# Kernel optimization log

Hardware: AMD Instinct MI355X
Metric: run time of the kernel (lower is better)

The kernel has to match this reference:

```python
import jax, jax.numpy as jnp
import numpy as np


def _mlp2(x, W1, b1, W2, b2):
    # two-layer MLP with ReLU hidden activation
    h = jax.nn.relu(jnp.einsum('...i,ij->...j', x, W1) + b1)
    return jnp.einsum('...i,ij->...j', h, W2) + b2


def setup_inputs() -> dict:
    key = jax.random.key(0)
    ks = jax.random.split(key, 8)
    B, N, D = 8, 256, 64
    positions = jax.random.normal(ks[0], (B, N, 3), dtype=jnp.float32)
    values = jax.random.normal(ks[1], (B, N, D), dtype=jnp.float32)
    # value_net: 2 -> D -> D ; score_net: D -> D -> 1 (He-style init)
    Wv1 = jax.random.normal(ks[2], (2, D), dtype=jnp.float32) * np.sqrt(2.0 / 2)
    bv1 = jnp.zeros((D,), dtype=jnp.float32)
    Wv2 = jax.random.normal(ks[3], (D, D), dtype=jnp.float32) * np.sqrt(2.0 / D)
    bv2 = jnp.zeros((D,), dtype=jnp.float32)
    Ws1 = jax.random.normal(ks[4], (D, D), dtype=jnp.float32) * np.sqrt(2.0 / D)
    bs1 = jnp.zeros((D,), dtype=jnp.float32)
    Ws2 = jax.random.normal(ks[5], (D, 1), dtype=jnp.float32) * np.sqrt(2.0 / D)
    bs2 = jnp.zeros((1,), dtype=jnp.float32)
    return dict(positions=positions, values=values, Wv1=Wv1, bv1=bv1, Wv2=Wv2,
                bv2=bv2, Ws1=Ws1, bs1=bs1, Ws2=Ws2, bs2=bs2)


def reference(positions, values, Wv1, bv1, Wv2, bv2, Ws1, bs1, Ws2, bs2):
    # rank-2 geometric algebra attention, reduce=True, merge_fun=join_fun='mean'
    B, N, _ = positions.shape
    r_i = positions[:, :, None, :]            # [B, N, 1, 3]
    r_j = positions[:, None, :, :]            # [B, 1, N, 3]
    # geometric product of two vectors -> scalar (dot) + bivector (wedge)
    dot = jnp.sum(r_i * r_j, axis=-1)         # [B, N, N] scalar part
    wedge = jnp.cross(r_i, r_j)               # [B, N, N, 3] bivector components
    biv_norm = jnp.sqrt(jnp.sum(wedge * wedge, axis=-1) + 1e-20)
    invariants = jnp.stack([dot, biv_norm], axis=-1)             # [B, N, N, 2]
    # merge_fun='mean' over the pair of node values
    merged = 0.5 * (values[:, :, None, :] + values[:, None, :, :])  # [B,N,N,D]
    invar_values = _mlp2(invariants, Wv1, bv1, Wv2, bv2)            # [B,N,N,D]
    # join_fun='mean' of value_net(invariants) and merged node values
    joined = 0.5 * (invar_values + merged)                          # [B,N,N,D]
    scores = _mlp2(joined, Ws1, bs1, Ws2, bs2)                      # [B,N,N,1]
    # reduce=True: softmax over all N*N product indices, output is [B, D]
    attn = jax.nn.softmax(scores.reshape(B, N * N), axis=-1).reshape(B, N, N, 1)
    output = jnp.sum(attn * joined, axis=(1, 2))                    # [B, D]
    return output
```

## Files before the change

kernel.cpp:

```cpp
#include <hip/hip_runtime.h>
#include <hip/hip_bf16.h>
#include <hip/hip_fp16.h>

#define NB 8
#define NN 256
#define DD 64

#define OFF_WCF   0
#define OFF_W1F   2048
#define OFF_CSF   4096
#define OFF_CC    5632
#define OFF_MI    5696
#define OFF_RSI   7744
#define OFF_SHR   9792
#define OFF_VF    140864

typedef __attribute__((ext_vector_type(4))) float f32x4;
typedef _Float16 f16x8 __attribute__((ext_vector_type(8)));

__global__ __launch_bounds__(256) void k_setup(
    const float* __restrict__ values, const float* __restrict__ Wv1,
    const float* __restrict__ bv1, const float* __restrict__ Wv2,
    const float* __restrict__ bv2, const float* __restrict__ Ws1,
    const float* __restrict__ bs1, float* __restrict__ ws)
{
    int idx = blockIdx.x * 256 + threadIdx.x;
    if (idx < 131072) {
        ((_Float16*)(ws + OFF_VF))[idx] = (_Float16)values[idx];
    } else if (idx < 135168) {
        int e = idx - 131072;
        int j = e & 7, ln = (e >> 3) & 63, nt = (e >> 9) & 3, ks = e >> 11;
        int k = ks * 32 + (ln >> 4) * 8 + j;
        int d = nt * 16 + (ln & 15);
        float s = 0.f;
#pragma unroll 8
        for (int m = 0; m < 64; m++) s = fmaf(Wv2[k * 64 + m], Ws1[m * 64 + d], s);
        ((_Float16*)(ws + OFF_WCF))[e] = (_Float16)(0.5f * s);
    } else if (idx < 139264) {
        int e = idx - 135168;
        int j = e & 7, ln = (e >> 3) & 63, nt = (e >> 9) & 3, ks = e >> 11;
        int k = ks * 32 + (ln >> 4) * 8 + j;
        int d = nt * 16 + (ln & 15);
        ((_Float16*)(ws + OFF_W1F))[e] = (_Float16)(0.25f * Ws1[k * 64 + d]);
    } else if (idx < 142336) {
        int e = idx - 139264;
        int ln = e / 48;
        int rem = e - ln * 48;
        int coef = rem >> 4, kslot = rem & 15;
        int ks = kslot >> 3, j = kslot & 7;
        int k = ks * 32 + (ln >> 4) * 8 + j;
        float v = (coef == 0) ? Wv1[k] : (coef == 1) ? Wv1[64 + k] : bv1[k];
        ((_Float16*)(ws + OFF_CSF))[ln * 48 + coef * 16 + kslot] = (_Float16)v;
    } else if (idx < 142400) {
        int d = idx - 142336;
        float s = 0.f;
#pragma unroll 8
        for (int k = 0; k < 64; k++) s = fmaf(bv2[k], Ws1[k * 64 + d], s);
        ws[OFF_CC + d] = 0.5f * s + bs1[d];
    }
}

__global__ __launch_bounds__(256, 4) void k_main(
    const float* __restrict__ pos, const float* __restrict__ Wv1,
    const float* __restrict__ bv1, const float* __restrict__ Ws2,
    float* __restrict__ ws)
{
    __shared__ float2   ldsDB[2 * 256];
    __shared__ float    ldsS[2][256];
    __shared__ float    ldsCCU[2 * 64];
    __shared__ float    ldsWs2[64];
    __shared__ float    ldsPos[6];
    __shared__ float    ldsRed[4];
    __shared__ float    ldsP[4][64];
    __shared__ _Float16 ldsW1[4096];

    int b  = blockIdx.x >> 7;
    int i0 = (blockIdx.x & 127) * 2;
    int t  = threadIdx.x;
    int lane = t & 63, wv = t >> 6;
    int q = lane >> 4, col = lane & 15;

    const _Float16* vf = (const _Float16*)(ws + OFF_VF);

    {
        const float4* src = (const float4*)(ws + OFF_W1F);
        float4* dst = (float4*)ldsW1;
        dst[t] = src[t];
        dst[256 + t] = src[256 + t];
    }
    if (t < 6)  ldsPos[t] = pos[(b * 256 + i0) * 3 + t];
    if (t < 64) ldsWs2[t] = Ws2[t];
    if (t < 128) ldsCCU[t] = ws[OFF_CC + (t & 63)];

    f16x8 cfA[2], cfB[2], cfC[2];
    {
        const f16x8* cs = (const f16x8*)((const _Float16*)(ws + OFF_CSF) + lane * 48);
        cfA[0] = cs[0]; cfA[1] = cs[1];
        cfB[0] = cs[2]; cfB[1] = cs[3];
        cfC[0] = cs[4]; cfC[1] = cs[5];
    }
    f16x8 wcf[2][4];
    {
        const f16x8* p = (const f16x8*)(ws + OFF_WCF);
#pragma unroll
        for (int ks = 0; ks < 2; ks++)
#pragma unroll
            for (int nt = 0; nt < 4; nt++)
                wcf[ks][nt] = p[(ks * 4 + nt) * 64 + lane];
    }
    __syncthreads();

    {
        float px = pos[(b * 256 + t) * 3 + 0];
        float py = pos[(b * 256 + t) * 3 + 1];
        float pz = pos[(b * 256 + t) * 3 + 2];
#pragma unroll
        for (int ii = 0; ii < 2; ii++) {
            float ax = ldsPos[ii * 3 + 0], ay = ldsPos[ii * 3 + 1], az = ldsPos[ii * 3 + 2];
            float dot = ax * px + ay * py + az * pz;
            float cx = ay * pz - az * py;
            float cy = az * px - ax * pz;
            float cz = ax * py - ay * px;
            float biv = sqrtf(cx * cx + cy * cy + cz * cz + 1e-20f);
            ldsDB[ii * 256 + t] = make_float2(dot, biv);
        }
    }

    if (wv == 0) {
        const f16x8* w1 = (const f16x8*)ldsW1;
        f16x8 afu[2];
#pragma unroll
        for (int ks = 0; ks < 2; ks++) {
            if (col < 2)
                afu[ks] = ((const f16x8*)(vf + (b * 256 + i0 + col) * 64))[ks * 4 + q];
            else
                afu[ks] = (f16x8)(_Float16)0.f;
        }
        f32x4 ua[4];
#pragma unroll
        for (int nt = 0; nt < 4; nt++) {
            ua[nt] = (f32x4){0.f, 0.f, 0.f, 0.f};
            ua[nt] = __builtin_amdgcn_mfma_f32_16x16x32_f16(afu[0], w1[(0 * 4 + nt) * 64 + lane], ua[nt], 0, 0, 0);
            ua[nt] = __builtin_amdgcn_mfma_f32_16x16x32_f16(afu[1], w1[(1 * 4 + nt) * 64 + lane], ua[nt], 0, 0, 0);
        }
        if (q == 0) {
#pragma unroll
            for (int nt = 0; nt < 4; nt++) {
#pragma unroll
                for (int r = 0; r < 2; r++)
                    ldsCCU[r * 64 + nt * 16 + col] += ua[nt][r];
            }
        }
    }
    __syncthreads();

    const f16x8* w1 = (const f16x8*)ldsW1;

#pragma unroll
    for (int jt4 = 0; jt4 < 4; jt4++) {
        int jt = wv * 4 + jt4;
        f16x8 av[2];
#pragma unroll
        for (int ks = 0; ks < 2; ks++)
            av[ks] = ((const f16x8*)(vf + (b * 256 + jt * 16 + col) * 64))[ks * 4 + q];

#pragma unroll
        for (int ii = 0; ii < 2; ii++) {
            float2 db = ldsDB[ii * 256 + jt * 16 + col];
            _Float16 dh = (_Float16)db.x, bh = (_Float16)db.y;
            f16x8 d8, b8;
#pragma unroll
            for (int p = 0; p < 8; p++) { d8[p] = dh; b8[p] = bh; }
            f16x8 af[2];
#pragma unroll
            for (int ks = 0; ks < 2; ks++) {
                f16x8 h = d8 * cfA[ks] + b8 * cfB[ks] + cfC[ks];
                af[ks] = __builtin_elementwise_max(h, (f16x8)(_Float16)0.f);
            }
            f32x4 acc[4];
#pragma unroll
            for (int nt = 0; nt < 4; nt++) {
                acc[nt] = (f32x4){0.f, 0.f, 0.f, 0.f};
                acc[nt] = __builtin_amdgcn_mfma_f32_16x16x32_f16(av[0], w1[(0 * 4 + nt) * 64 + lane], acc[nt], 0, 0, 0);
                acc[nt] = __builtin_amdgcn_mfma_f32_16x16x32_f16(av[1], w1[(1 * 4 + nt) * 64 + lane], acc[nt], 0, 0, 0);
                acc[nt] = __builtin_amdgcn_mfma_f32_16x16x32_f16(af[0], wcf[0][nt], acc[nt], 0, 0, 0);
                acc[nt] = __builtin_amdgcn_mfma_f32_16x16x32_f16(af[1], wcf[1][nt], acc[nt], 0, 0, 0);
            }
            float tr[4] = {0.f, 0.f, 0.f, 0.f};
#pragma unroll
            for (int nt = 0; nt < 4; nt++) {
                float cu = ldsCCU[ii * 64 + nt * 16 + col];
                float w2 = ldsWs2[nt * 16 + col];
#pragma unroll
                for (int r = 0; r < 4; r++) {
                    float s = acc[nt][r] + cu;
                    tr[r] = fmaf(fmaxf(s, 0.f), w2, tr[r]);
                }
            }
#pragma unroll
            for (int m = 1; m < 16; m <<= 1) {
#pragma unroll
                for (int r = 0; r < 4; r++) tr[r] += __shfl_xor(tr[r], m);
            }
            if (col == 0) {
                float4 sc4 = make_float4(tr[0], tr[1], tr[2], tr[3]);
                *(float4*)&ldsS[ii][jt * 16 + q * 4] = sc4;
            }
        }
    }
    __syncthreads();

    float A = Wv1[lane], B = Wv1[64 + lane], C = bv1[lane];
#pragma unroll
    for (int ii = 0; ii < 2; ii++) {
        float sv = ldsS[ii][t];
        float wm = sv;
#pragma unroll
        for (int md = 1; md < 64; md <<= 1) wm = fmaxf(wm, __shfl_xor(wm, md));
        if (lane == 0) ldsRed[wv] = wm;
        __syncthreads();
        float m_row = fmaxf(fmaxf(ldsRed[0], ldsRed[1]), fmaxf(ldsRed[2], ldsRed[3]));
        float wgt = __expf(sv - m_row);
        float rsp = wgt;
#pragma unroll
        for (int md = 1; md < 64; md <<= 1) rsp += __shfl_xor(rsp, md);
        ldsS[ii][t] = wgt;
        __syncthreads();
        if (lane == 0) ldsRed[wv] = rsp;
        __syncthreads();
        float rowsum = ldsRed[0] + ldsRed[1] + ldsRed[2] + ldsRed[3];

        float acc = 0.f;
#pragma unroll 8
        for (int jj = 0; jj < 64; jj++) {
            int j = wv * 64 + jj;
            float w = ldsS[ii][j];
            float2 db = ldsDB[ii * 256 + j];
            float h = fmaxf(fmaf(db.x, A, fmaf(db.y, B, C)), 0.f);
            acc = fmaf(w, h, acc);
        }
        ldsP[wv][lane] = acc;
        __syncthreads();
        int row = b * 256 + i0 + ii;
        if (t < 64)
            ws[OFF_SHR + row * 64 + t] = ldsP[0][t] + ldsP[1][t] + ldsP[2][t] + ldsP[3][t];
        if (t == 0) { ws[OFF_MI + row] = m_row; ws[OFF_RSI + row] = rowsum; }
        __syncthreads();
    }
}

__global__ __launch_bounds__(256) void k_final(
    const float* __restrict__ values, const float* __restrict__ Wv2,
    const float* __restrict__ bv2, const float* __restrict__ ws,
    float* __restrict__ out)
{
    __shared__ float scl[256], zl[256], red[4], pS[4][64], pA[4][64], shv[64], a2v[64];
    int b = blockIdx.x, t = threadIdx.x, wv = t >> 6, lane = t & 63;

    float mi = ws[OFF_MI + b * 256 + t];
    float wm = mi;
#pragma unroll
    for (int md = 1; md < 64; md <<= 1) wm = fmaxf(wm, __shfl_xor(wm, md));
    if (lane == 0) red[wv] = wm;
    __syncthreads();
    float M = fmaxf(fmaxf(red[0], red[1]), fmaxf(red[2], red[3]));

    float rs = ws[OFF_RSI + b * 256 + t];
    float sc = __expf(mi - M);
    float zt = sc * rs;
    scl[t] = sc; zl[t] = zt;
    float zp = zt;
#pragma unroll
    for (int md = 1; md < 64; md <<= 1) zp += __shfl_xor(zp, md);
    __syncthreads();
    if (lane == 0) red[wv] = zp;
    __syncthreads();
    float Z = red[0] + red[1] + red[2] + red[3];

    float accS = 0.f, accA = 0.f;
    const float* shrB = ws + OFF_SHR + b * 256 * 64;
    const float* vB   = values + b * 256 * 64;
#pragma unroll 4
    for (int jj = 0; jj < 64; jj++) {
        int row = wv * 64 + jj;
        accS = fmaf(scl[row], shrB[row * 64 + lane], accS);
        accA = fmaf(zl[row],  vB[row * 64 + lane],  accA);
    }
    pS[wv][lane] = accS; pA[wv][lane] = accA;
    __syncthreads();
    if (t < 64) {
        shv[t] = pS[0][t] + pS[1][t] + pS[2][t] + pS[3][t];
        a2v[t] = pA[0][t] + pA[1][t] + pA[2][t] + pA[3][t];
    }
    __syncthreads();
    if (t < 64) {
        float t1 = 0.f;
#pragma unroll 8
        for (int k = 0; k < 64; k++) t1 = fmaf(shv[k], Wv2[k * 64 + t], t1);
        out[b * 64 + t] = 0.5f * (t1 + a2v[t]) / Z + 0.5f * bv2[t];
    }
}

extern "C" void kernel_launch(void* const* d_in, const int* in_sizes, int n_in,
                              void* d_out, int out_size, void* d_ws, size_t ws_size,
                              hipStream_t stream)
{
    const float* positions = (const float*)d_in[0];
    const float* values    = (const float*)d_in[1];
    const float* Wv1       = (const float*)d_in[2];
    const float* bv1       = (const float*)d_in[3];
    const float* Wv2       = (const float*)d_in[4];
    const float* bv2       = (const float*)d_in[5];
    const float* Ws1       = (const float*)d_in[6];
    const float* bs1       = (const float*)d_in[7];
    const float* Ws2       = (const float*)d_in[8];
    float* ws  = (float*)d_ws;
    float* out = (float*)d_out;

    k_setup<<<557, 256, 0, stream>>>(values, Wv1, bv1, Wv2, bv2, Ws1, bs1, ws);
    k_main<<<1024, 256, 0, stream>>>(positions, Wv1, bv1, Ws2, ws);
    k_final<<<NB, 256, 0, stream>>>(values, Wv2, bv2, ws, out);
}
```

Baseline: 105.6 us.

## Fuse final reduction into main kernel and convert values to fp16 in place

Stops pre-converting the values tensor to fp16 in the setup kernel. The main kernel now loads fp32 values directly and converts them in registers, which shrinks the setup grid. The separate final kernel is removed: each batch's last-finishing block, found with an atomic counter and threadfence, does the softmax normalisation and output projection. This saves one launch and the fp16 staging buffer, at the cost of reading twice as many bytes for values in the main loop plus extra LDS and atomics.

```diff
diff --git a/kernel.cpp b/kernel.cpp
--- a/kernel.cpp
+++ b/kernel.cpp
@@ -10,25 +10,32 @@
 #define OFF_W1F   2048
 #define OFF_CSF   4096
 #define OFF_CC    5632
-#define OFF_MI    5696
-#define OFF_RSI   7744
-#define OFF_SHR   9792
-#define OFF_VF    140864
+#define OFF_CNT   5696
+#define OFF_MI    5704
+#define OFF_RSI   7752
+#define OFF_SHR   9800
 
 typedef __attribute__((ext_vector_type(4))) float f32x4;
 typedef _Float16 f16x8 __attribute__((ext_vector_type(8)));
 
+static __device__ __forceinline__ f16x8 cvt8(const float* __restrict__ p) {
+    float4 a = *(const float4*)p;
+    float4 c = *(const float4*)(p + 4);
+    f16x8 r;
+    r[0] = (_Float16)a.x; r[1] = (_Float16)a.y; r[2] = (_Float16)a.z; r[3] = (_Float16)a.w;
+    r[4] = (_Float16)c.x; r[5] = (_Float16)c.y; r[6] = (_Float16)c.z; r[7] = (_Float16)c.w;
+    return r;
+}
+
 __global__ __launch_bounds__(256) void k_setup(
-    const float* __restrict__ values, const float* __restrict__ Wv1,
-    const float* __restrict__ bv1, const float* __restrict__ Wv2,
-    const float* __restrict__ bv2, const float* __restrict__ Ws1,
-    const float* __restrict__ bs1, float* __restrict__ ws)
+    const float* __restrict__ Wv1, const float* __restrict__ bv1,
+    const float* __restrict__ Wv2, const float* __restrict__ bv2,
+    const float* __restrict__ Ws1, const float* __restrict__ bs1,
+    float* __restrict__ ws)
 {
     int idx = blockIdx.x * 256 + threadIdx.x;
-    if (idx < 131072) {
-        ((_Float16*)(ws + OFF_VF))[idx] = (_Float16)values[idx];
-    } else if (idx < 135168) {
-        int e = idx - 131072;
+    if (idx < 4096) {
+        int e = idx;
         int j = e & 7, ln = (e >> 3) & 63, nt = (e >> 9) & 3, ks = e >> 11;
         int k = ks * 32 + (ln >> 4) * 8 + j;
         int d = nt * 16 + (ln & 15);
@@ -36,14 +43,14 @@
 #pragma unroll 8
         for (int m = 0; m < 64; m++) s = fmaf(Wv2[k * 64 + m], Ws1[m * 64 + d], s);
         ((_Float16*)(ws + OFF_WCF))[e] = (_Float16)(0.5f * s);
-    } else if (idx < 139264) {
-        int e = idx - 135168;
+    } else if (idx < 8192) {
+        int e = idx - 4096;
         int j = e & 7, ln = (e >> 3) & 63, nt = (e >> 9) & 3, ks = e >> 11;
         int k = ks * 32 + (ln >> 4) * 8 + j;
         int d = nt * 16 + (ln & 15);
         ((_Float16*)(ws + OFF_W1F))[e] = (_Float16)(0.25f * Ws1[k * 64 + d]);
-    } else if (idx < 142336) {
-        int e = idx - 139264;
+    } else if (idx < 11264) {
+        int e = idx - 8192;
         int ln = e / 48;
         int rem = e - ln * 48;
         int coef = rem >> 4, kslot = rem & 15;
@@ -51,19 +58,23 @@
         int k = ks * 32 + (ln >> 4) * 8 + j;
         float v = (coef == 0) ? Wv1[k] : (coef == 1) ? Wv1[64 + k] : bv1[k];
         ((_Float16*)(ws + OFF_CSF))[ln * 48 + coef * 16 + kslot] = (_Float16)v;
-    } else if (idx < 142400) {
-        int d = idx - 142336;
+    } else if (idx < 11328) {
+        int d = idx - 11264;
         float s = 0.f;
 #pragma unroll 8
         for (int k = 0; k < 64; k++) s = fmaf(bv2[k], Ws1[k * 64 + d], s);
         ws[OFF_CC + d] = 0.5f * s + bs1[d];
+    } else if (idx < 11336) {
+        ((unsigned*)(ws + OFF_CNT))[idx - 11328] = 0u;
     }
 }
 
 __global__ __launch_bounds__(256, 4) void k_main(
-    const float* __restrict__ pos, const float* __restrict__ Wv1,
-    const float* __restrict__ bv1, const float* __restrict__ Ws2,
-    float* __restrict__ ws)
+    const float* __restrict__ pos, const float* __restrict__ values,
+    const float* __restrict__ Wv1, const float* __restrict__ bv1,
+    const float* __restrict__ Wv2, const float* __restrict__ bv2,
+    const float* __restrict__ Ws2, float* __restrict__ ws,
+    float* __restrict__ out)
 {
     __shared__ float2   ldsDB[2 * 256];
     __shared__ float    ldsS[2][256];
@@ -73,14 +84,14 @@
     __shared__ float    ldsRed[4];
     __shared__ float    ldsP[4][64];
     __shared__ _Float16 ldsW1[4096];
+    __shared__ float    fscl[256], fzl[256], fred[4], fpS[4][64], fpA[4][64], fshv[64], fa2v[64];
+    __shared__ unsigned s_last;
 
     int b  = blockIdx.x >> 7;
     int i0 = (blockIdx.x & 127) * 2;
     int t  = threadIdx.x;
     int lane = t & 63, wv = t >> 6;
     int q = lane >> 4, col = lane & 15;
-
-    const _Float16* vf = (const _Float16*)(ws + OFF_VF);
 
     {
         const float4* src = (const float4*)(ws + OFF_W1F);
@@ -132,7 +143,7 @@
 #pragma unroll
         for (int ks = 0; ks < 2; ks++) {
             if (col < 2)
-                afu[ks] = ((const f16x8*)(vf + (b * 256 + i0 + col) * 64))[ks * 4 + q];
+                afu[ks] = cvt8(values + (b * 256 + i0 + col) * 64 + ks * 32 + q * 8);
             else
                 afu[ks] = (f16x8)(_Float16)0.f;
         }
@@ -162,7 +173,7 @@
         f16x8 av[2];
 #pragma unroll
         for (int ks = 0; ks < 2; ks++)
-            av[ks] = ((const f16x8*)(vf + (b * 256 + jt * 16 + col) * 64))[ks * 4 + q];
+            av[ks] = cvt8(values + (b * 256 + jt * 16 + col) * 64 + ks * 32 + q * 8);
 
 #pragma unroll
         for (int ii = 0; ii < 2; ii++) {
@@ -247,57 +258,58 @@
         if (t == 0) { ws[OFF_MI + row] = m_row; ws[OFF_RSI + row] = rowsum; }
         __syncthreads();
     }
-}
-
-__global__ __launch_bounds__(256) void k_final(
-    const float* __restrict__ values, const float* __restrict__ Wv2,
-    const float* __restrict__ bv2, const float* __restrict__ ws,
-    float* __restrict__ out)
-{
-    __shared__ float scl[256], zl[256], red[4], pS[4][64], pA[4][64], shv[64], a2v[64];
-    int b = blockIdx.x, t = threadIdx.x, wv = t >> 6, lane = t & 63;
-
-    float mi = ws[OFF_MI + b * 256 + t];
-    float wm = mi;
-#pragma unroll
-    for (int md = 1; md < 64; md <<= 1) wm = fmaxf(wm, __shfl_xor(wm, md));
-    if (lane == 0) red[wv] = wm;
+
+    __threadfence();
+    if (t == 0) {
+        unsigned old = __hip_atomic_fetch_add((unsigned*)(ws + OFF_CNT) + b, 1u,
+                                              __ATOMIC_ACQ_REL, __HIP_MEMORY_SCOPE_AGENT);
+        s_last = (old == 127u) ? 1u : 0u;
+    }
     __syncthreads();
-    float M = fmaxf(fmaxf(red[0], red[1]), fmaxf(red[2], red[3]));
-
-    float rs = ws[OFF_RSI + b * 256 + t];
-    float sc = __expf(mi - M);
-    float zt = sc * rs;
-    scl[t] = sc; zl[t] = zt;
-    float zp = zt;
-#pragma unroll
-    for (int md = 1; md < 64; md <<= 1) zp += __shfl_xor(zp, md);
-    __syncthreads();
-    if (lane == 0) red[wv] = zp;
-    __syncthreads();
-    float Z = red[0] + red[1] + red[2] + red[3];
-
-    float accS = 0.f, accA = 0.f;
-    const float* shrB = ws + OFF_SHR + b * 256 * 64;
-    const float* vB   = values + b * 256 * 64;
+    if (s_last) {
+        __threadfence();
+        float mi = ws[OFF_MI + b * 256 + t];
+        float wm = mi;
+#pragma unroll
+        for (int md = 1; md < 64; md <<= 1) wm = fmaxf(wm, __shfl_xor(wm, md));
+        if (lane == 0) fred[wv] = wm;
+        __syncthreads();
+        float M = fmaxf(fmaxf(fred[0], fred[1]), fmaxf(fred[2], fred[3]));
+
+        float rs = ws[OFF_RSI + b * 256 + t];
+        float sc = __expf(mi - M);
+        float zt = sc * rs;
+        fscl[t] = sc; fzl[t] = zt;
+        float zp = zt;
+#pragma unroll
+        for (int md = 1; md < 64; md <<= 1) zp += __shfl_xor(zp, md);
+        __syncthreads();
+        if (lane == 0) fred[wv] = zp;
+        __syncthreads();
+        float Z = fred[0] + fred[1] + fred[2] + fred[3];
+
+        float accS = 0.f, accA = 0.f;
+        const float* shrB = ws + OFF_SHR + b * 256 * 64;
+        const float* vB   = values + b * 256 * 64;
 #pragma unroll 4
-    for (int jj = 0; jj < 64; jj++) {
-        int row = wv * 64 + jj;
-        accS = fmaf(scl[row], shrB[row * 64 + lane], accS);
-        accA = fmaf(zl[row],  vB[row * 64 + lane],  accA);
-    }
-    pS[wv][lane] = accS; pA[wv][lane] = accA;
-    __syncthreads();
-    if (t < 64) {
-        shv[t] = pS[0][t] + pS[1][t] + pS[2][t] + pS[3][t];
-        a2v[t] = pA[0][t] + pA[1][t] + pA[2][t] + pA[3][t];
-    }
-    __syncthreads();
-    if (t < 64) {
-        float t1 = 0.f;
+        for (int jj = 0; jj < 64; jj++) {
+            int row = wv * 64 + jj;
+            accS = fmaf(fscl[row], shrB[row * 64 + lane], accS);
+            accA = fmaf(fzl[row],  vB[row * 64 + lane],  accA);
+        }
+        fpS[wv][lane] = accS; fpA[wv][lane] = accA;
+        __syncthreads();
+        if (t < 64) {
+            fshv[t] = fpS[0][t] + fpS[1][t] + fpS[2][t] + fpS[3][t];
+            fa2v[t] = fpA[0][t] + fpA[1][t] + fpA[2][t] + fpA[3][t];
+        }
+        __syncthreads();
+        if (t < 64) {
+            float t1 = 0.f;
 #pragma unroll 8
-        for (int k = 0; k < 64; k++) t1 = fmaf(shv[k], Wv2[k * 64 + t], t1);
-        out[b * 64 + t] = 0.5f * (t1 + a2v[t]) / Z + 0.5f * bv2[t];
+            for (int k = 0; k < 64; k++) t1 = fmaf(fshv[k], Wv2[k * 64 + t], t1);
+            out[b * 64 + t] = 0.5f * (t1 + fa2v[t]) / Z + 0.5f * bv2[t];
+        }
     }
 }
 
@@ -317,7 +329,6 @@
     float* ws  = (float*)d_ws;
     float* out = (float*)d_out;
 
-    k_setup<<<557, 256, 0, stream>>>(values, Wv1, bv1, Wv2, bv2, Ws1, bs1, ws);
-    k_main<<<1024, 256, 0, stream>>>(positions, Wv1, bv1, Ws2, ws);
-    k_final<<<NB, 256, 0, stream>>>(values, Wv2, bv2, ws, out);
+    k_setup<<<45, 256, 0, stream>>>(Wv1, bv1, Wv2, bv2, Ws1, bs1, ws);
+    k_main<<<1024, 256, 0, stream>>>(positions, values, Wv1, bv1, Wv2, bv2, Ws2, ws, out);
 }
```

Measured after the change: 185.0 us. 1.75x slower.

## Read fp32 values directly in main kernel, one row per block, prefetch tiles

Applied to the files above, without the earlier changes.

Removes the fp16 pre-conversion of values from the setup kernel and instead loads fp32 values in k_main, converting to fp16 in registers and software-prefetching the next j-tile. Each block now handles one row i instead of two, doubling the grid to 2048 blocks. The per-row u-term MFMA is computed by every wave and broadcast with a shuffle, which removes one block barrier. Softmax barriers are also trimmed. The cost is that the V@W1 MFMA is recomputed per row (no reuse across the two rows) and values are read at twice the width from global/L2.

```diff
diff --git a/kernel.cpp b/kernel.cpp
--- a/kernel.cpp
+++ b/kernel.cpp
@@ -10,25 +10,29 @@
 #define OFF_W1F   2048
 #define OFF_CSF   4096
 #define OFF_CC    5632
-#define OFF_MI    5696
-#define OFF_RSI   7744
-#define OFF_SHR   9792
-#define OFF_VF    140864
+#define OFF_MI    5704
+#define OFF_RSI   7752
+#define OFF_SHR   9800
 
 typedef __attribute__((ext_vector_type(4))) float f32x4;
 typedef _Float16 f16x8 __attribute__((ext_vector_type(8)));
 
+static __device__ __forceinline__ f16x8 cvt2(float4 a, float4 c) {
+    f16x8 r;
+    r[0] = (_Float16)a.x; r[1] = (_Float16)a.y; r[2] = (_Float16)a.z; r[3] = (_Float16)a.w;
+    r[4] = (_Float16)c.x; r[5] = (_Float16)c.y; r[6] = (_Float16)c.z; r[7] = (_Float16)c.w;
+    return r;
+}
+
 __global__ __launch_bounds__(256) void k_setup(
-    const float* __restrict__ values, const float* __restrict__ Wv1,
-    const float* __restrict__ bv1, const float* __restrict__ Wv2,
-    const float* __restrict__ bv2, const float* __restrict__ Ws1,
-    const float* __restrict__ bs1, float* __restrict__ ws)
+    const float* __restrict__ Wv1, const float* __restrict__ bv1,
+    const float* __restrict__ Wv2, const float* __restrict__ bv2,
+    const float* __restrict__ Ws1, const float* __restrict__ bs1,
+    float* __restrict__ ws)
 {
     int idx = blockIdx.x * 256 + threadIdx.x;
-    if (idx < 131072) {
-        ((_Float16*)(ws + OFF_VF))[idx] = (_Float16)values[idx];
-    } else if (idx < 135168) {
-        int e = idx - 131072;
+    if (idx < 4096) {
+        int e = idx;
         int j = e & 7, ln = (e >> 3) & 63, nt = (e >> 9) & 3, ks = e >> 11;
         int k = ks * 32 + (ln >> 4) * 8 + j;
         int d = nt * 16 + (ln & 15);
@@ -36,14 +40,14 @@
 #pragma unroll 8
         for (int m = 0; m < 64; m++) s = fmaf(Wv2[k * 64 + m], Ws1[m * 64 + d], s);
         ((_Float16*)(ws + OFF_WCF))[e] = (_Float16)(0.5f * s);
-    } else if (idx < 139264) {
-        int e = idx - 135168;
+    } else if (idx < 8192) {
+        int e = idx - 4096;
         int j = e & 7, ln = (e >> 3) & 63, nt = (e >> 9) & 3, ks = e >> 11;
         int k = ks * 32 + (ln >> 4) * 8 + j;
         int d = nt * 16 + (ln & 15);
         ((_Float16*)(ws + OFF_W1F))[e] = (_Float16)(0.25f * Ws1[k * 64 + d]);
-    } else if (idx < 142336) {
-        int e = idx - 139264;
+    } else if (idx < 11264) {
+        int e = idx - 8192;
         int ln = e / 48;
         int rem = e - ln * 48;
         int coef = rem >> 4, kslot = rem & 15;
@@ -51,8 +55,8 @@
         int k = ks * 32 + (ln >> 4) * 8 + j;
         float v = (coef == 0) ? Wv1[k] : (coef == 1) ? Wv1[64 + k] : bv1[k];
         ((_Float16*)(ws + OFF_CSF))[ln * 48 + coef * 16 + kslot] = (_Float16)v;
-    } else if (idx < 142400) {
-        int d = idx - 142336;
+    } else if (idx < 11328) {
+        int d = idx - 11264;
         float s = 0.f;
 #pragma unroll 8
         for (int k = 0; k < 64; k++) s = fmaf(bv2[k], Ws1[k * 64 + d], s);
@@ -61,26 +65,40 @@
 }
 
 __global__ __launch_bounds__(256, 4) void k_main(
-    const float* __restrict__ pos, const float* __restrict__ Wv1,
-    const float* __restrict__ bv1, const float* __restrict__ Ws2,
-    float* __restrict__ ws)
+    const float* __restrict__ pos, const float* __restrict__ values,
+    const float* __restrict__ Wv1, const float* __restrict__ bv1,
+    const float* __restrict__ Ws2, float* __restrict__ ws)
 {
-    __shared__ float2   ldsDB[2 * 256];
-    __shared__ float    ldsS[2][256];
-    __shared__ float    ldsCCU[2 * 64];
+    __shared__ float2   ldsDB[256];
+    __shared__ float    ldsS[256];
+    __shared__ float    ldsCC[64];
     __shared__ float    ldsWs2[64];
-    __shared__ float    ldsPos[6];
-    __shared__ float    ldsRed[4];
+    __shared__ float    ldsPos[3];
+    __shared__ float    ldsRedM[4];
+    __shared__ float    ldsRedS[4];
     __shared__ float    ldsP[4][64];
     __shared__ _Float16 ldsW1[4096];
 
-    int b  = blockIdx.x >> 7;
-    int i0 = (blockIdx.x & 127) * 2;
-    int t  = threadIdx.x;
+    int b = blockIdx.x >> 8;
+    int i = blockIdx.x & 255;
+    int t = threadIdx.x;
     int lane = t & 63, wv = t >> 6;
     int q = lane >> 4, col = lane & 15;
 
-    const _Float16* vf = (const _Float16*)(ws + OFF_VF);
+    const float* vB = values + b * (NN * DD);
+
+    float4 nf0, nf1, nf2, nf3;
+    {
+        const float* p = vB + (wv * 64 + col) * 64 + q * 8;
+        nf0 = *(const float4*)p;        nf1 = *(const float4*)(p + 4);
+        nf2 = *(const float4*)(p + 32); nf3 = *(const float4*)(p + 36);
+    }
+    float4 vi0 = {0,0,0,0}, vi1 = {0,0,0,0}, vi2 = {0,0,0,0}, vi3 = {0,0,0,0};
+    if (col == 0) {
+        const float* p = vB + i * 64 + q * 8;
+        vi0 = *(const float4*)p;        vi1 = *(const float4*)(p + 4);
+        vi2 = *(const float4*)(p + 32); vi3 = *(const float4*)(p + 36);
+    }
 
     {
         const float4* src = (const float4*)(ws + OFF_W1F);
@@ -88,9 +106,9 @@
         dst[t] = src[t];
         dst[256 + t] = src[256 + t];
     }
-    if (t < 6)  ldsPos[t] = pos[(b * 256 + i0) * 3 + t];
-    if (t < 64) ldsWs2[t] = Ws2[t];
-    if (t < 128) ldsCCU[t] = ws[OFF_CC + (t & 63)];
+    if (t < 3)  ldsPos[t] = pos[(b * 256 + i) * 3 + t];
+    if (t >= 64 && t < 128) ldsCC[t - 64] = ws[OFF_CC + t - 64];
+    if (t >= 128 && t < 192) ldsWs2[t - 128] = Ws2[t - 128];
 
     f16x8 cfA[2], cfB[2], cfC[2];
     {
@@ -114,138 +132,119 @@
         float px = pos[(b * 256 + t) * 3 + 0];
         float py = pos[(b * 256 + t) * 3 + 1];
         float pz = pos[(b * 256 + t) * 3 + 2];
-#pragma unroll
-        for (int ii = 0; ii < 2; ii++) {
-            float ax = ldsPos[ii * 3 + 0], ay = ldsPos[ii * 3 + 1], az = ldsPos[ii * 3 + 2];
-            float dot = ax * px + ay * py + az * pz;
-            float cx = ay * pz - az * py;
-            float cy = az * px - ax * pz;
-            float cz = ax * py - ay * px;
-            float biv = sqrtf(cx * cx + cy * cy + cz * cz + 1e-20f);
-            ldsDB[ii * 256 + t] = make_float2(dot, biv);
-        }
-    }
-
-    if (wv == 0) {
-        const f16x8* w1 = (const f16x8*)ldsW1;
-        f16x8 afu[2];
-#pragma unroll
-        for (int ks = 0; ks < 2; ks++) {
-            if (col < 2)
-                afu[ks] = ((const f16x8*)(vf + (b * 256 + i0 + col) * 64))[ks * 4 + q];
-            else
-                afu[ks] = (f16x8)(_Float16)0.f;
-        }
-        f32x4 ua[4];
+        float ax = ldsPos[0], ay = ldsPos[1], az = ldsPos[2];
+        float dot = ax * px + ay * py + az * pz;
+        float cx = ay * pz - az * py;
+        float cy = az * px - ax * pz;
+        float cz = ax * py - ay * px;
+        float biv = sqrtf(cx * cx + cy * cy + cz * cz + 1e-20f);
+        ldsDB[t] = make_float2(dot, biv);
+    }
+
+    const f16x8* w1 = (const f16x8*)ldsW1;
+
+    float cu[4], w2r[4];
+    {
+        f16x8 afu0 = cvt2(vi0, vi1);
+        f16x8 afu1 = cvt2(vi2, vi3);
 #pragma unroll
         for (int nt = 0; nt < 4; nt++) {
-            ua[nt] = (f32x4){0.f, 0.f, 0.f, 0.f};
-            ua[nt] = __builtin_amdgcn_mfma_f32_16x16x32_f16(afu[0], w1[(0 * 4 + nt) * 64 + lane], ua[nt], 0, 0, 0);
-            ua[nt] = __builtin_amdgcn_mfma_f32_16x16x32_f16(afu[1], w1[(1 * 4 + nt) * 64 + lane], ua[nt], 0, 0, 0);
-        }
-        if (q == 0) {
-#pragma unroll
-            for (int nt = 0; nt < 4; nt++) {
-#pragma unroll
-                for (int r = 0; r < 2; r++)
-                    ldsCCU[r * 64 + nt * 16 + col] += ua[nt][r];
-            }
-        }
-    }
-    __syncthreads();
-
-    const f16x8* w1 = (const f16x8*)ldsW1;
+            f32x4 ua = (f32x4){0.f, 0.f, 0.f, 0.f};
+            ua = __builtin_amdgcn_mfma_f32_16x16x32_f16(afu0, w1[(0 * 4 + nt) * 64 + lane], ua, 0, 0, 0);
+            ua = __builtin_amdgcn_mfma_f32_16x16x32_f16(afu1, w1[(1 * 4 + nt) * 64 + lane], ua, 0, 0, 0);
+            cu[nt] = ldsCC[nt * 16 + col] + __shfl(ua[0], col);
+            w2r[nt] = ldsWs2[nt * 16 + col];
+        }
+    }
 
 #pragma unroll
     for (int jt4 = 0; jt4 < 4; jt4++) {
         int jt = wv * 4 + jt4;
-        f16x8 av[2];
-#pragma unroll
-        for (int ks = 0; ks < 2; ks++)
-            av[ks] = ((const f16x8*)(vf + (b * 256 + jt * 16 + col) * 64))[ks * 4 + q];
-
-#pragma unroll
-        for (int ii = 0; ii < 2; ii++) {
-            float2 db = ldsDB[ii * 256 + jt * 16 + col];
-            _Float16 dh = (_Float16)db.x, bh = (_Float16)db.y;
-            f16x8 d8, b8;
-#pragma unroll
-            for (int p = 0; p < 8; p++) { d8[p] = dh; b8[p] = bh; }
-            f16x8 af[2];
-#pragma unroll
-            for (int ks = 0; ks < 2; ks++) {
-                f16x8 h = d8 * cfA[ks] + b8 * cfB[ks] + cfC[ks];
-                af[ks] = __builtin_elementwise_max(h, (f16x8)(_Float16)0.f);
+        f16x8 av0 = cvt2(nf0, nf1);
+        f16x8 av1 = cvt2(nf2, nf3);
+        if (jt4 < 3) {
+            const float* p = vB + ((jt + 1) * 16 + col) * 64 + q * 8;
+            nf0 = *(const float4*)p;        nf1 = *(const float4*)(p + 4);
+            nf2 = *(const float4*)(p + 32); nf3 = *(const float4*)(p + 36);
+        }
+
+        f32x4 acc[4];
+#pragma unroll
+        for (int nt = 0; nt < 4; nt++) {
+            acc[nt] = (f32x4){0.f, 0.f, 0.f, 0.f};
+            acc[nt] = __builtin_amdgcn_mfma_f32_16x16x32_f16(av0, w1[(0 * 4 + nt) * 64 + lane], acc[nt], 0, 0, 0);
+            acc[nt] = __builtin_amdgcn_mfma_f32_16x16x32_f16(av1, w1[(1 * 4 + nt) * 64 + lane], acc[nt], 0, 0, 0);
+        }
+
+        float2 db = ldsDB[jt * 16 + col];
+        _Float16 dh = (_Float16)db.x, bh = (_Float16)db.y;
+        f16x8 d8, b8;
+#pragma unroll
+        for (int p = 0; p < 8; p++) { d8[p] = dh; b8[p] = bh; }
+        f16x8 af0, af1;
+        {
+            f16x8 h0 = d8 * cfA[0] + b8 * cfB[0] + cfC[0];
+            f16x8 h1 = d8 * cfA[1] + b8 * cfB[1] + cfC[1];
+            af0 = __builtin_elementwise_max(h0, (f16x8)(_Float16)0.f);
+            af1 = __builtin_elementwise_max(h1, (f16x8)(_Float16)0.f);
+        }
+#pragma unroll
+        for (int nt = 0; nt < 4; nt++) {
+            acc[nt] = __builtin_amdgcn_mfma_f32_16x16x32_f16(af0, wcf[0][nt], acc[nt], 0, 0, 0);
+            acc[nt] = __builtin_amdgcn_mfma_f32_16x16x32_f16(af1, wcf[1][nt], acc[nt], 0, 0, 0);
+        }
+
+        float tr[4] = {0.f, 0.f, 0.f, 0.f};
+#pragma unroll
+        for (int nt = 0; nt < 4; nt++) {
+#pragma unroll
+            for (int r = 0; r < 4; r++) {
+                float s = acc[nt][r] + cu[nt];
+                tr[r] = fmaf(fmaxf(s, 0.f), w2r[nt], tr[r]);
             }
-            f32x4 acc[4];
-#pragma unroll
-            for (int nt = 0; nt < 4; nt++) {
-                acc[nt] = (f32x4){0.f, 0.f, 0.f, 0.f};
-                acc[nt] = __builtin_amdgcn_mfma_f32_16x16x32_f16(av[0], w1[(0 * 4 + nt) * 64 + lane], acc[nt], 0, 0, 0);
-                acc[nt] = __builtin_amdgcn_mfma_f32_16x16x32_f16(av[1], w1[(1 * 4 + nt) * 64 + lane], acc[nt], 0, 0, 0);
-                acc[nt] = __builtin_amdgcn_mfma_f32_16x16x32_f16(af[0], wcf[0][nt], acc[nt], 0, 0, 0);
-                acc[nt] = __builtin_amdgcn_mfma_f32_16x16x32_f16(af[1], wcf[1][nt], acc[nt], 0, 0, 0);
-            }
-            float tr[4] = {0.f, 0.f, 0.f, 0.f};
-#pragma unroll
-            for (int nt = 0; nt < 4; nt++) {
-                float cu = ldsCCU[ii * 64 + nt * 16 + col];
-                float w2 = ldsWs2[nt * 16 + col];
-#pragma unroll
-                for (int r = 0; r < 4; r++) {
-                    float s = acc[nt][r] + cu;
-                    tr[r] = fmaf(fmaxf(s, 0.f), w2, tr[r]);
-                }
-            }
-#pragma unroll
-            for (int m = 1; m < 16; m <<= 1) {
-#pragma unroll
-                for (int r = 0; r < 4; r++) tr[r] += __shfl_xor(tr[r], m);
-            }
-            if (col == 0) {
-                float4 sc4 = make_float4(tr[0], tr[1], tr[2], tr[3]);
-                *(float4*)&ldsS[ii][jt * 16 + q * 4] = sc4;
-            }
-        }
-    }
-    __syncthreads();
+        }
+#pragma unroll
+        for (int m = 1; m < 16; m <<= 1) {
+#pragma unroll
+            for (int r = 0; r < 4; r++) tr[r] += __shfl_xor(tr[r], m);
+        }
+        if (col == 0)
+            *(float4*)&ldsS[jt * 16 + q * 4] = make_float4(tr[0], tr[1], tr[2], tr[3]);
+    }
+
+    float sv = ldsS[t];
+    float wm = sv;
+#pragma unroll
+    for (int md = 1; md < 64; md <<= 1) wm = fmaxf(wm, __shfl_xor(wm, md));
+    if (lane == 0) ldsRedM[wv] = wm;
+    __syncthreads();
+    float m_row = fmaxf(fmaxf(ldsRedM[0], ldsRedM[1]), fmaxf(ldsRedM[2], ldsRedM[3]));
+    float wgt = __expf(sv - m_row);
+    float rsp = wgt;
+#pragma unroll
+    for (int md = 1; md < 64; md <<= 1) rsp += __shfl_xor(rsp, md);
+    ldsS[t] = wgt;
+    if (lane == 0) ldsRedS[wv] = rsp;
+    __syncthreads();
+    float rowsum = ldsRedS[0] + ldsRedS[1] + ldsRedS[2] + ldsRedS[3];
 
     float A = Wv1[lane], B = Wv1[64 + lane], C = bv1[lane];
-#pragma unroll
-    for (int ii = 0; ii < 2; ii++) {
-        float sv = ldsS[ii][t];
-        float wm = sv;
-#pragma unroll
-        for (int md = 1; md < 64; md <<= 1) wm = fmaxf(wm, __shfl_xor(wm, md));
-        if (lane == 0) ldsRed[wv] = wm;
-        __syncthreads();
-        float m_row = fmaxf(fmaxf(ldsRed[0], ldsRed[1]), fmaxf(ldsRed[2], ldsRed[3]));
-        float wgt = __expf(sv - m_row);
-        float rsp = wgt;
-#pragma unroll
-        for (int md = 1; md < 64; md <<= 1) rsp += __shfl_xor(rsp, md);
-        ldsS[ii][t] = wgt;
-        __syncthreads();
-        if (lane == 0) ldsRed[wv] = rsp;
-        __syncthreads();
-        float rowsum = ldsRed[0] + ldsRed[1] + ldsRed[2] + ldsRed[3];
-
-        float acc = 0.f;
+    float acc = 0.f;
 #pragma unroll 8
-        for (int jj = 0; jj < 64; jj++) {
-            int j = wv * 64 + jj;
-            float w = ldsS[ii][j];
-            float2 db = ldsDB[ii * 256 + j];
-            float h = fmaxf(fmaf(db.x, A, fmaf(db.y, B, C)), 0.f);
-            acc = fmaf(w, h, acc);
-        }
-        ldsP[wv][lane] = acc;
-        __syncthreads();
-        int row = b * 256 + i0 + ii;
-        if (t < 64)
-            ws[OFF_SHR + row * 64 + t] = ldsP[0][t] + ldsP[1][t] + ldsP[2][t] + ldsP[3][t];
-        if (t == 0) { ws[OFF_MI + row] = m_row; ws[OFF_RSI + row] = rowsum; }
-        __syncthreads();
+    for (int jj = 0; jj < 64; jj++) {
+        int j = wv * 64 + jj;
+        float w = ldsS[j];
+        float2 db = ldsDB[j];
+        float h = fmaxf(fmaf(db.x, A, fmaf(db.y, B, C)), 0.f);
+        acc = fmaf(w, h, acc);
+    }
+    ldsP[wv][lane] = acc;
+    __syncthreads();
+    if (t < 64)
+        ws[OFF_SHR + (b * 256 + i) * 64 + t] = ldsP[0][t] + ldsP[1][t] + ldsP[2][t] + ldsP[3][t];
+    if (t == 0) {
+        ws[OFF_MI  + b * 256 + i] = m_row;
+        ws[OFF_RSI + b * 256 + i] = rowsum;
     }
 }
 
@@ -317,7 +316,7 @@
     float* ws  = (float*)d_ws;
     float* out = (float*)d_out;
 
-    k_setup<<<557, 256, 0, stream>>>(values, Wv1, bv1, Wv2, bv2, Ws1, bs1, ws);
-    k_main<<<1024, 256, 0, stream>>>(positions, Wv1, bv1, Ws2, ws);
+    k_setup<<<45, 256, 0, stream>>>(Wv1, bv1, Wv2, bv2, Ws1, bs1, ws);
+    k_main<<<2048, 256, 0, stream>>>(positions, values, Wv1, bv1, Ws2, ws);
     k_final<<<NB, 256, 0, stream>>>(values, Wv2, bv2, ws, out);
 }
```

Measured after the change: 107.5 us. No clear change (+1.8%).
